# Performance work log

Hardware: AMD Instinct MI355X
Metric: run time of the kernel (lower is better)

The kernel has to match this reference:

```python
import jax, jax.numpy as jnp
import numpy as np

D = 1024       # num_feature == heads*dim_head
NHEADS = 16
HD = 64
INNER = NHEADS * HD
FF = 2048      # hardcoded mlp_dim in CSGO_model
L = 4          # depth
NOUT = 26      # hardcoded number of InvDynamic heads
IDH = 512      # inverse_dynamic_dim
B = 64
T = 32         # horizon


def _ln(x, g=None, b=None, eps=1e-5):
    mu = jnp.mean(x, axis=-1, keepdims=True)
    var = jnp.mean((x - mu) ** 2, axis=-1, keepdims=True)
    y = (x - mu) * jax.lax.rsqrt(var + eps)
    if g is not None:
        y = y * g + b
    return y


def setup_inputs() -> dict:
    key = jax.random.key(0)
    ks = jax.random.split(key, 20)
    s = 0.02
    inp = {
        'x': jax.random.normal(ks[0], (B, T, D), jnp.float32),
        # transformer params, stacked over depth L
        'qkv_w': jax.random.normal(ks[1], (L, D, 3 * INNER), jnp.float32) * s,
        'out_w': jax.random.normal(ks[2], (L, INNER, D), jnp.float32) * s,
        'out_b': jnp.zeros((L, D), jnp.float32),
        'attn_ln_g': jnp.ones((L, D), jnp.float32),
        'attn_ln_b': jnp.zeros((L, D), jnp.float32),
        'ff_ln_g': jnp.ones((L, D), jnp.float32),
        'ff_ln_b': jnp.zeros((L, D), jnp.float32),
        'ff_w1': jax.random.normal(ks[3], (L, D, FF), jnp.float32) * s,
        'ff_b1': jnp.zeros((L, FF), jnp.float32),
        'ff_w2': jax.random.normal(ks[4], (L, FF, D), jnp.float32) * s,
        'ff_b2': jnp.zeros((L, D), jnp.float32),
        # 26 InvDynamic heads, stacked
        'head_w1': jax.random.normal(ks[5], (NOUT, 2 * D, IDH), jnp.float32) * s,
        'head_b1': jnp.zeros((NOUT, IDH), jnp.float32),
        'head_w2': jax.random.normal(ks[6], (NOUT, IDH, IDH), jnp.float32) * s,
        'head_b2': jnp.zeros((NOUT, IDH), jnp.float32),
        'head_w3': jax.random.normal(ks[7], (NOUT, IDH, 1), jnp.float32) * s,
        'head_b3': jnp.zeros((NOUT, 1), jnp.float32),
    }
    return inp


def _forward(x, qkv_w, out_w, out_b, attn_ln_g, attn_ln_b, ff_ln_g, ff_ln_b,
             ff_w1, ff_b1, ff_w2, ff_b2,
             head_w1, head_b1, head_w2, head_b2, head_w3, head_b3):
    scale = HD ** -0.5

    def block(h, p):
        (qw, ow, ob, ag, ab, fg, fb, w1, b1, w2, b2) = p
        # x = attn(prenorm_ln(mid_ln(x))) + x  (mid LayerNorm has no affine, eps=1e-6)
        y = _ln(h, eps=1e-6)
        y = _ln(y, ag, ab)
        qkv = y @ qw                               # [B,T,3*INNER]
        q, k, v = jnp.split(qkv, 3, axis=-1)
        def split_heads(t):
            return t.reshape(t.shape[0], t.shape[1], NHEADS, HD).transpose(0, 2, 1, 3)
        q, k, v = split_heads(q), split_heads(k), split_heads(v)
        attn = jax.nn.softmax(jnp.einsum('bhqd,bhkd->bhqk', q, k) * scale, axis=-1)
        o = jnp.einsum('bhqk,bhkd->bhqd', attn, v)
        o = o.transpose(0, 2, 1, 3).reshape(h.shape[0], h.shape[1], INNER)
        h = h + (o @ ow + ob)
        # x = ff(prenorm_ln(x)) + x
        y = _ln(h, fg, fb)
        y = jax.nn.gelu(y @ w1 + b1, approximate=False) @ w2 + b2
        return h + y, None

    params = (qkv_w, out_w, out_b, attn_ln_g, attn_ln_b, ff_ln_g, ff_ln_b,
              ff_w1, ff_b1, ff_w2, ff_b2)
    x, _ = jax.lax.scan(block, x, params)

    # x_comb = concat(x[:,0], x[:,1])  -> [B, 2D]
    x_comb = jnp.concatenate([x[:, 0, :], x[:, 1, :]], axis=1)
    # 26 independent 3-layer MLP heads, batched as grouped GEMMs
    h1 = jax.nn.relu(jnp.einsum('bd,ndk->bnk', x_comb, head_w1) + head_b1)
    h2 = jax.nn.relu(jnp.einsum('bnk,nkj->bnj', h1, head_w2) + head_b2)
    out = jnp.einsum('bnk,nkj->bnj', h2, head_w3) + head_b3   # [B,26,1]
    return out


def reference(x, qkv_w, out_w, out_b, attn_ln_g, attn_ln_b, ff_ln_g, ff_ln_b,
              ff_w1, ff_b1, ff_w2, ff_b2,
              head_w1, head_b1, head_w2, head_b2, head_w3, head_b3):
    return _forward(x, qkv_w, out_w, out_b, attn_ln_g, attn_ln_b, ff_ln_g,
                    ff_ln_b, ff_w1, ff_b1, ff_w2, ff_b2,
                    head_w1, head_b1, head_w2, head_b2, head_w3, head_b3)
```

## Files before the change

kernel.cpp:

```cpp
#include <hip/hip_runtime.h>
#include <math.h>

static constexpr int BATCH = 64;
static constexpr int SEQ   = 32;
static constexpr int TOK   = BATCH * SEQ;
static constexpr int DIM   = 1024;
static constexpr int NH    = 16;
static constexpr int HDIM  = 64;
static constexpr int FFD   = 2048;
static constexpr int LAYERS= 4;
static constexpr int NHEAD_OUT = 26;
static constexpr int IDH   = 512;

typedef __bf16 bf16_t;
typedef __bf16 bf16x4 __attribute__((ext_vector_type(4)));
typedef __bf16 bf16x8 __attribute__((ext_vector_type(8)));
typedef float  f32x4  __attribute__((ext_vector_type(4)));
typedef float  f32x16 __attribute__((ext_vector_type(16)));
typedef unsigned short us4 __attribute__((ext_vector_type(4)));
typedef unsigned short us8 __attribute__((ext_vector_type(8)));

__device__ __forceinline__ unsigned short f2bfu(float f) {
    return __builtin_bit_cast(unsigned short, (bf16_t)f);
}

__device__ __forceinline__ void gload_lds16(const void* gp, void* lp) {
    __builtin_amdgcn_global_load_lds(
        (const __attribute__((address_space(1))) unsigned int*)gp,
        (__attribute__((address_space(3))) unsigned int*)lp,
        16, 0, 0);
}

__device__ __forceinline__ void tx_chunks4(const float* __restrict__ src,
                                           bf16_t* __restrict__ dst,
                                           int K, int N, int base4) {
    int nkb = K >> 6;
    int kk = threadIdx.x >> 6;
    int l  = threadIdx.x & 63;
    int nl = l & 31, k8 = (l >> 5) * 8;
    int base = base4 * 4;
    #pragma unroll
    for (int q = 0; q < 4; ++q) {
        int chunk = base + q;
        int ns = chunk / nkb;
        int kt = chunk - ns * nkb;
        int n = ns * 32 + nl;
        int kb = kt * 64 + kk * 16 + k8;
        us8 o;
        #pragma unroll
        for (int j = 0; j < 8; ++j)
            o[j] = f2bfu(src[(long)(kb + j) * N + n]);
        *(us8*)(dst + (long)chunk * 2048 + kk * 512 + l * 8) = o;
    }
}

__global__ __launch_bounds__(256) void txd1(const float* __restrict__ src,
                                            bf16_t* __restrict__ dst,
                                            int K, int N) {
    tx_chunks4(src, dst, K, N, blockIdx.x);
}

__device__ __forceinline__ float block_sum(float v, float* red) {
    #pragma unroll
    for (int off = 32; off > 0; off >>= 1) v += __shfl_down(v, off);
    int lane = threadIdx.x & 63;
    int w    = threadIdx.x >> 6;
    if (lane == 0) red[w] = v;
    __syncthreads();
    float t = red[0] + red[1] + red[2] + red[3];
    __syncthreads();
    return t;
}

template<bool PRE, bool F32IN>
__global__ __launch_bounds__(256) void ln_kernel(const void* __restrict__ xv,
                                                 const float* __restrict__ g,
                                                 const float* __restrict__ b,
                                                 bf16_t* __restrict__ y,
                                                 bf16_t* __restrict__ hout) {
    __shared__ float red[4];
    long row = blockIdx.x;
    int tid = threadIdx.x;
    float4 v;
    if (F32IN) {
        const float* xr = (const float*)xv + row * DIM;
        v = *(const float4*)(xr + tid * 4);
        us4 hc;
        hc.x = f2bfu(v.x); hc.y = f2bfu(v.y); hc.z = f2bfu(v.z); hc.w = f2bfu(v.w);
        *(us4*)(hout + row * DIM + tid * 4) = hc;
        v.x = (float)(bf16_t)v.x; v.y = (float)(bf16_t)v.y;
        v.z = (float)(bf16_t)v.z; v.w = (float)(bf16_t)v.w;
    } else {
        const bf16_t* xr = (const bf16_t*)xv + row * DIM;
        bf16x4 r4 = *(const bf16x4*)(xr + tid * 4);
        v.x = (float)r4[0]; v.y = (float)r4[1]; v.z = (float)r4[2]; v.w = (float)r4[3];
    }
    if (PRE) {
        float s  = block_sum(v.x + v.y + v.z + v.w, red);
        float mu = s * (1.0f / DIM);
        v.x -= mu; v.y -= mu; v.z -= mu; v.w -= mu;
        float ss = block_sum(v.x*v.x + v.y*v.y + v.z*v.z + v.w*v.w, red);
        float r  = 1.0f / sqrtf(ss * (1.0f / DIM) + 1e-6f);
        v.x *= r; v.y *= r; v.z *= r; v.w *= r;
    }
    float s  = block_sum(v.x + v.y + v.z + v.w, red);
    float mu = s * (1.0f / DIM);
    v.x -= mu; v.y -= mu; v.z -= mu; v.w -= mu;
    float ss = block_sum(v.x*v.x + v.y*v.y + v.z*v.z + v.w*v.w, red);
    float r  = 1.0f / sqrtf(ss * (1.0f / DIM) + 1e-5f);
    float4 gg = *(const float4*)(g + tid * 4);
    float4 bb = *(const float4*)(b + tid * 4);
    us4 o;
    o.x = f2bfu(v.x * r * gg.x + bb.x);
    o.y = f2bfu(v.y * r * gg.y + bb.y);
    o.z = f2bfu(v.z * r * gg.z + bb.z);
    o.w = f2bfu(v.w * r * gg.w + bb.w);
    *(us4*)(y + row * DIM + tid * 4) = o;
}

template<int BM, int BN, int WM, int WN, int EPI>
__global__ __launch_bounds__(256) void gemm32(
    const bf16_t* __restrict__ A, const bf16_t* __restrict__ BT,
    const float* __restrict__ bias, const bf16_t* __restrict__ resid,
    bf16_t* __restrict__ Ch,
    int N, int K, int gemmBlocks, int gx,
    const float* __restrict__ txsrc, bf16_t* __restrict__ txdst,
    int txK, int txN)
{
    constexpr int WAVES_N = BN / WN;
    constexpr int FM = WM / 32, FN = WN / 32;
    constexpr int NSTG = BM / 32 + BN / 32;

    __shared__ bf16_t As[2][BM * 64];
    __shared__ bf16_t Bs[2][BN * 64];

    int bid = blockIdx.x;
    if (bid >= gemmBlocks) {
        tx_chunks4(txsrc, txdst, txK, txN, bid - gemmBlocks);
        return;
    }
    int bx = bid % gx, by = bid / gx;

    int tid  = threadIdx.x;
    int wave = tid >> 6, lane = tid & 63;
    int wr = wave / WAVES_N, wc = wave % WAVES_N;
    int m0 = by * BM, n0 = bx * BN;

    f32x16 acc[FM][FN];
    #pragma unroll
    for (int m = 0; m < FM; ++m)
        #pragma unroll
        for (int n = 0; n < FN; ++n)
            #pragma unroll
            for (int r = 0; r < 16; ++r)
                acc[m][n][r] = 0.f;

    long rsb = (long)K * 2;
    int  lr  = lane & 31;
    int  lkb = (lane >> 5) * 16;
    int  nkb = K >> 6;

    const char* Abase = (const char*)A + (long)(m0 + lr) * rsb + lkb;
    const char* Bbase = (const char*)BT + (long)(n0 >> 5) * nkb * 4096 + lane * 16;

    auto stage = [&](int c, int t) {
        long kb = (long)t * 128;
        #pragma unroll
        for (int i = 0; i < BM / 32; ++i) {
            int b = i * 4 + wave;
            gload_lds16(Abase + (long)(b >> 2) * 32 * rsb + (b & 3) * 32 + kb,
                        (char*)&As[c][0] + b * 1024);
        }
        #pragma unroll
        for (int i = 0; i < BN / 32; ++i) {
            int b = i * 4 + wave;
            gload_lds16(Bbase + ((long)(b >> 2) * nkb + t) * 4096 + (b & 3) * 1024,
                        (char*)&Bs[c][0] + b * 1024);
        }
    };

    int nt = K >> 6;
    stage(0, 0);
    int cur = 0;
    for (int t = 0; t < nt; ++t) {
        if (t + 1 < nt) {
            stage(cur ^ 1, t + 1);
            asm volatile("s_waitcnt vmcnt(%c0)" :: "i"(NSTG) : "memory");
        } else {
            asm volatile("s_waitcnt vmcnt(0)" ::: "memory");
        }
        __builtin_amdgcn_s_barrier();
        asm volatile("" ::: "memory");
        bf16x8 af[FM][4], bq[FN][4];
        #pragma unroll
        for (int m = 0; m < FM; ++m)
            #pragma unroll
            for (int kk = 0; kk < 4; ++kk)
                af[m][kk] = *(const bf16x8*)((const char*)&As[cur][0] +
                            ((wr * FM + m) * 4 + kk) * 1024 + (lane << 4));
        #pragma unroll
        for (int n = 0; n < FN; ++n)
            #pragma unroll
            for (int kk = 0; kk < 4; ++kk)
                bq[n][kk] = *(const bf16x8*)((const char*)&Bs[cur][0] +
                            ((wc * FN + n) * 4 + kk) * 1024 + (lane << 4));
        #pragma unroll
        for (int kk = 0; kk < 4; ++kk)
            #pragma unroll
            for (int m = 0; m < FM; ++m)
                #pragma unroll
                for (int n = 0; n < FN; ++n)
                    acc[m][n] = __builtin_amdgcn_mfma_f32_32x32x16_bf16(
                        af[m][kk], bq[n][kk], acc[m][n], 0, 0, 0);
        asm volatile("" ::: "memory");
        __builtin_amdgcn_s_barrier();
        cur ^= 1;
    }

    int rbase = 4 * (lane >> 5);
    #pragma unroll
    for (int m = 0; m < FM; ++m) {
        #pragma unroll
        for (int n = 0; n < FN; ++n) {
            int colI = n0 + wc * WN + n * 32 + (lane & 31);
            float bb = (EPI != 0) ? bias[colI] : 0.f;
            #pragma unroll
            for (int r = 0; r < 16; ++r) {
                int rowI = m0 + wr * WM + m * 32 + rbase + (r & 3) + 8 * (r >> 2);
                float v = acc[m][n][r] + bb;
                if (EPI == 2) v = 0.5f * v * (1.0f + erff(v * 0.70710678118654752f));
                long off = (long)rowI * N + colI;
                if (EPI == 1) v += (float)resid[off];
                Ch[off] = (bf16_t)v;
            }
        }
    }
}

__global__ __launch_bounds__(256) void gemm_hd(
    const bf16_t* __restrict__ A, const float* __restrict__ Bw,
    const float* __restrict__ bias, bf16_t* __restrict__ C,
    int N, int K, long aStride, long sA, long sB, long sbias, long sC)
{
    long g = blockIdx.z;
    A += g * sA;
    const float* Bp = Bw + g * sB;
    bias += g * sbias;
    bf16_t* Cp = C + g * sC;

    __shared__ bf16_t As[2][64 * 64];
    __shared__ float  Bf[2][64 * 64];

    int tid = threadIdx.x, wave = tid >> 6, lane = tid & 63;
    int wr = wave >> 1, wc = wave & 1;
    int n0 = blockIdx.x * 64;

    f32x4 acc[2][2];
    #pragma unroll
    for (int m = 0; m < 2; ++m)
        #pragma unroll
        for (int n = 0; n < 2; ++n)
            acc[m][n] = f32x4{0.f, 0.f, 0.f, 0.f};

    long rsb = aStride * 2;
    int  lr  = lane & 15;
    int  lkb = (lane >> 4) * 16;
    const char* Abase = (const char*)A + (long)lr * rsb + lkb;

    auto stage = [&](int c, int t) {
        long kb = (long)t * 128;
        #pragma unroll
        for (int i = 0; i < 2; ++i) {
            int b = i * 4 + wave;
            gload_lds16(Abase + (long)(b >> 1) * 16 * rsb + (b & 1) * 64 + kb,
                        (char*)&As[c][0] + b * 1024);
        }
        #pragma unroll
        for (int i = 0; i < 4; ++i) {
            int ch = i * 4 + wave;
            int row = ch * 4 + (lane >> 4);
            gload_lds16((const char*)Bp + ((long)(t * 64 + row) * N + n0) * 4 + (lane & 15) * 16,
                        (char*)&Bf[c][0] + ch * 1024);
        }
    };

    int nt = K >> 6;
    stage(0, 0);
    int cur = 0;
    for (int t = 0; t < nt; ++t) {
        if (t + 1 < nt) {
            stage(cur ^ 1, t + 1);
            asm volatile("s_waitcnt vmcnt(6)" ::: "memory");
        } else {
            asm volatile("s_waitcnt vmcnt(0)" ::: "memory");
        }
        __builtin_amdgcn_s_barrier();
        asm volatile("" ::: "memory");
        bf16x8 af[2][2], bq[2][2];
        #pragma unroll
        for (int m = 0; m < 2; ++m)
            #pragma unroll
            for (int h = 0; h < 2; ++h)
                af[m][h] = *(const bf16x8*)((const char*)&As[cur][0] +
                           ((wr * 2 + m) * 2 + h) * 1024 + (lane << 4));
        #pragma unroll
        for (int n = 0; n < 2; ++n) {
            int nl = wc * 32 + n * 16 + lr;
            #pragma unroll
            for (int h = 0; h < 2; ++h) {
                #pragma unroll
                for (int j = 0; j < 8; ++j) {
                    float v = Bf[cur][(h * 32 + (lane >> 4) * 8 + j) * 64 + nl];
                    bq[n][h][j] = (bf16_t)v;
                }
            }
        }
        #pragma unroll
        for (int h = 0; h < 2; ++h)
            #pragma unroll
            for (int m = 0; m < 2; ++m)
                #pragma unroll
                for (int n = 0; n < 2; ++n)
                    acc[m][n] = __builtin_amdgcn_mfma_f32_16x16x32_bf16(
                        af[m][h], bq[n][h], acc[m][n], 0, 0, 0);
        asm volatile("" ::: "memory");
        __builtin_amdgcn_s_barrier();
        cur ^= 1;
    }

    int lq = (lane >> 4) * 4;
    #pragma unroll
    for (int m = 0; m < 2; ++m) {
        #pragma unroll
        for (int n = 0; n < 2; ++n) {
            int colI = n0 + wc * 32 + n * 16 + lr;
            float bb = bias[colI];
            #pragma unroll
            for (int j = 0; j < 4; ++j) {
                int rowI = wr * 32 + m * 16 + lq + j;
                float v = fmaxf(acc[m][n][j] + bb, 0.0f);
                Cp[(long)rowI * N + colI] = (bf16_t)v;
            }
        }
    }
}

__global__ __launch_bounds__(256) void attn_kernel(const bf16_t* __restrict__ qkv,
                                                   bf16_t* __restrict__ o) {
    int bh = blockIdx.x;
    int b  = bh >> 4;
    int hh = bh & 15;
    __shared__ float qs[32][65];
    __shared__ float kt[64][36];
    __shared__ float vs[32][68];
    __shared__ float ps[32][33];
    const bf16_t* base = qkv + (long)b * SEQ * (3 * DIM) + hh * HDIM;
    int tid = threadIdx.x;

    {
        int t = tid >> 3, c = (tid & 7) * 8;
        bf16x8 qv = *(const bf16x8*)(base + (long)t * 3 * DIM + c);
        bf16x8 kv = *(const bf16x8*)(base + (long)t * 3 * DIM + DIM + c);
        bf16x8 vv = *(const bf16x8*)(base + (long)t * 3 * DIM + 2 * DIM + c);
        #pragma unroll
        for (int j = 0; j < 8; ++j) {
            int d = c + j;
            qs[t][d] = (float)qv[j];
            kt[d][(((t >> 2) ^ ((d >> 2) & 7)) << 2) + (t & 3)] = (float)kv[j];
            vs[t][d] = (float)vv[j];
        }
    }
    __syncthreads();

    {
        int r  = tid >> 3;
        int c0 = (tid & 7) * 4;
        f32x4 acc = {0.f, 0.f, 0.f, 0.f};
        #pragma unroll
        for (int d = 0; d < 64; ++d) {
            float qv = qs[r][d];
            float4 kv = *(const float4*)&kt[d][(((c0 >> 2) ^ ((d >> 2) & 7)) << 2)];
            acc[0] = fmaf(qv, kv.x, acc[0]);
            acc[1] = fmaf(qv, kv.y, acc[1]);
            acc[2] = fmaf(qv, kv.z, acc[2]);
            acc[3] = fmaf(qv, kv.w, acc[3]);
        }
        #pragma unroll
        for (int i = 0; i < 4; ++i) ps[r][c0 + i] = acc[i] * 0.125f;
    }
    __syncthreads();

    if (tid < 32) {
        float mx = -1e30f;
        for (int c = 0; c < 32; ++c) mx = fmaxf(mx, ps[tid][c]);
        float sum = 0.f;
        for (int c = 0; c < 32; ++c) { float e = expf(ps[tid][c] - mx); ps[tid][c] = e; sum += e; }
        float inv = 1.f / sum;
        for (int c = 0; c < 32; ++c) ps[tid][c] *= inv;
    }
    __syncthreads();

    {
        int r  = tid >> 3;
        int d0 = (tid & 7) * 8;
        float acc[8] = {};
        #pragma unroll
        for (int c = 0; c < 32; ++c) {
            float pv = ps[r][c];
            float4 v0 = *(const float4*)&vs[c][d0];
            float4 v1 = *(const float4*)&vs[c][d0 + 4];
            acc[0] = fmaf(pv, v0.x, acc[0]);
            acc[1] = fmaf(pv, v0.y, acc[1]);
            acc[2] = fmaf(pv, v0.z, acc[2]);
            acc[3] = fmaf(pv, v0.w, acc[3]);
            acc[4] = fmaf(pv, v1.x, acc[4]);
            acc[5] = fmaf(pv, v1.y, acc[5]);
            acc[6] = fmaf(pv, v1.z, acc[6]);
            acc[7] = fmaf(pv, v1.w, acc[7]);
        }
        us8 ov;
        #pragma unroll
        for (int j = 0; j < 8; ++j) ov[j] = f2bfu(acc[j]);
        *(us8*)(o + (long)b * SEQ * DIM + (long)r * DIM + hh * HDIM + d0) = ov;
    }
}

__global__ __launch_bounds__(256) void head3_kernel(const bf16_t* __restrict__ h2,
                                                    const float* __restrict__ w3,
                                                    const float* __restrict__ b3,
                                                    float* __restrict__ out) {
    int gid  = blockIdx.x * 256 + threadIdx.x;
    int wave = gid >> 6;
    int lane = gid & 63;
    if (wave >= NHEAD_OUT * BATCH) return;
    int n = wave >> 6;
    int b = wave & 63;
    const bf16_t* a = h2 + ((long)n * BATCH + b) * IDH;
    const float*  w = w3 + (long)n * IDH;
    float acc = 0.f;
    #pragma unroll
    for (int i = lane; i < IDH; i += 64) acc = fmaf((float)a[i], w[i], acc);
    #pragma unroll
    for (int off = 32; off > 0; off >>= 1) acc += __shfl_down(acc, off);
    if (lane == 0) out[b * NHEAD_OUT + n] = acc + b3[n];
}

extern "C" void kernel_launch(void* const* d_in, const int* in_sizes, int n_in,
                              void* d_out, int out_size, void* d_ws, size_t ws_size,
                              hipStream_t stream) {
    const float* x      = (const float*)d_in[0];
    const float* qkv_w  = (const float*)d_in[1];
    const float* out_w  = (const float*)d_in[2];
    const float* out_b  = (const float*)d_in[3];
    const float* attn_g = (const float*)d_in[4];
    const float* attn_b = (const float*)d_in[5];
    const float* ff_g   = (const float*)d_in[6];
    const float* ff_b   = (const float*)d_in[7];
    const float* ff_w1  = (const float*)d_in[8];
    const float* ff_b1  = (const float*)d_in[9];
    const float* ff_w2  = (const float*)d_in[10];
    const float* ff_b2  = (const float*)d_in[11];
    const float* hw1    = (const float*)d_in[12];
    const float* hb1    = (const float*)d_in[13];
    const float* hw2    = (const float*)d_in[14];
    const float* hb2    = (const float*)d_in[15];
    const float* hw3    = (const float*)d_in[16];
    const float* hb3    = (const float*)d_in[17];
    float* out = (float*)d_out;

    char* p = (char*)d_ws;
    bf16_t* h     = (bf16_t*)p;           p += (long)TOK * DIM * 2;
    bf16_t* qkvb  = (bf16_t*)p;           p += (long)TOK * 3 * DIM * 2;
    bf16_t* y     = (bf16_t*)p;           p += (long)TOK * DIM * 2;
    bf16_t* ob    = (bf16_t*)p;           p += (long)TOK * DIM * 2;
    bf16_t* ffb   = (bf16_t*)p;           p += (long)TOK * FFD * 2;
    bf16_t* h1    = (bf16_t*)p;           p += (long)NHEAD_OUT * BATCH * IDH * 2;
    bf16_t* h2    = (bf16_t*)p;           p += (long)NHEAD_OUT * BATCH * IDH * 2;
    bf16_t* qkvwt = (bf16_t*)p;           p += (long)LAYERS * DIM * 3 * DIM * 2;
    bf16_t* outwt = (bf16_t*)p;           p += (long)LAYERS * DIM * DIM * 2;
    bf16_t* ff1t  = (bf16_t*)p;           p += (long)LAYERS * DIM * FFD * 2;
    bf16_t* ff2t  = (bf16_t*)p;           p += (long)LAYERS * FFD * DIM * 2;

    const long sQ = (long)DIM * 3 * DIM;
    const long sO = (long)DIM * DIM;
    const long sF1 = (long)DIM * FFD;
    const long sF2 = (long)FFD * DIM;
    const int tbQ  = (3 * DIM / 32) * (DIM / 64) / 4;
    const int tbO  = (DIM / 32) * (DIM / 64) / 4;
    const int tbF1 = (FFD / 32) * (DIM / 64) / 4;
    const int tbF2 = (DIM / 32) * (FFD / 64) / 4;

    txd1<<<tbQ, 256, 0, stream>>>(qkv_w, qkvwt, DIM, 3 * DIM);

    for (int l = 0; l < LAYERS; ++l) {
        bool more = (l + 1 < LAYERS);
        if (l == 0)
            ln_kernel<true, true><<<TOK, 256, 0, stream>>>(
                x, attn_g, attn_b, y, h);
        else
            ln_kernel<true, false><<<TOK, 256, 0, stream>>>(
                h, attn_g + l * DIM, attn_b + l * DIM, y, nullptr);

        {
            int gx = 3 * DIM / 128, gb = gx * (TOK / 64);
            gemm32<64, 128, 32, 64, 0><<<gb + tbO, 256, 0, stream>>>(
                y, qkvwt + l * sQ, nullptr, nullptr, qkvb,
                3 * DIM, DIM, gb, gx,
                out_w + l * sO, outwt + l * sO, DIM, DIM);
        }
        attn_kernel<<<BATCH * NH, 256, 0, stream>>>(qkvb, ob);
        {
            int gx = DIM / 64, gb = gx * (TOK / 64);
            gemm32<64, 64, 32, 32, 1><<<gb + tbF1, 256, 0, stream>>>(
                ob, outwt + l * sO, out_b + l * DIM, h, h,
                DIM, DIM, gb, gx,
                ff_w1 + l * sF1, ff1t + l * sF1, DIM, FFD);
        }
        ln_kernel<false, false><<<TOK, 256, 0, stream>>>(
            h, ff_g + l * DIM, ff_b + l * DIM, y, nullptr);
        {
            int gx = FFD / 128, gb = gx * (TOK / 64);
            gemm32<64, 128, 32, 64, 2><<<gb + tbF2, 256, 0, stream>>>(
                y, ff1t + l * sF1, ff_b1 + l * FFD, nullptr, ffb,
                FFD, DIM, gb, gx,
                ff_w2 + l * sF2, ff2t + l * sF2, FFD, DIM);
        }
        {
            int gx = DIM / 64, gb = gx * (TOK / 64);
            gemm32<64, 64, 32, 32, 1><<<gb + (more ? tbQ : 0), 256, 0, stream>>>(
                ffb, ff2t + l * sF2, ff_b2 + l * DIM, h, h,
                DIM, FFD, gb, gx,
                qkv_w + (l + 1) * sQ, qkvwt + (l + 1) * sQ, DIM, 3 * DIM);
        }
    }

    gemm_hd<<<dim3(IDH / 64, 1, NHEAD_OUT), 256, 0, stream>>>(
        h, hw1, hb1, h1,
        IDH, 2 * DIM, (long)SEQ * DIM,
        0, (long)2 * DIM * IDH, IDH, (long)BATCH * IDH);
    gemm_hd<<<dim3(IDH / 64, 1, NHEAD_OUT), 256, 0, stream>>>(
        h1, hw2, hb2, h2,
        IDH, IDH, IDH,
        (long)BATCH * IDH, (long)IDH * IDH, IDH, (long)BATCH * IDH);
    head3_kernel<<<(NHEAD_OUT * BATCH * 64) / 256, 256, 0, stream>>>(h2, hw3, hb3, out);
}
```

Measured before the change: 515.0 us.

## Pre-convert head weights to bf16 in spare blocks of transformer GEMM launches

Adds extra blocks to each transformer GEMM launch that convert the fp32 InvDynamic head weights (w1, w2) to bf16 in chunks, spread across the 16 launches. The head GEMMs then stream bf16 weights, which halves their global and LDS traffic and removes the in-loop float-to-bf16 conversion. The conversion is still done every call, but it overlaps with the GEMM tails. It adds workspace and more blocks per GEMM launch, which could delay the GEMMs.

```diff
diff --git a/kernel.cpp b/kernel.cpp
--- a/kernel.cpp
+++ b/kernel.cpp
@@ -12,6 +12,9 @@
 static constexpr int NHEAD_OUT = 26;
 static constexpr int IDH   = 512;
 
+static constexpr int HB1 = (NHEAD_OUT * 2 * DIM * IDH) / 8192;
+static constexpr int HB2 = (NHEAD_OUT * IDH * IDH) / 8192;
+
 typedef __bf16 bf16_t;
 typedef __bf16 bf16x4 __attribute__((ext_vector_type(4)));
 typedef __bf16 bf16x8 __attribute__((ext_vector_type(8)));
@@ -51,6 +54,22 @@
         for (int j = 0; j < 8; ++j)
             o[j] = f2bfu(src[(long)(kb + j) * N + n]);
         *(us8*)(dst + (long)chunk * 2048 + kk * 512 + l * 8) = o;
+    }
+}
+
+__device__ __forceinline__ void cvt_chunk8k(const float* __restrict__ src,
+                                            bf16_t* __restrict__ dst,
+                                            int blk) {
+    long base = (long)blk * 8192 + threadIdx.x * 8;
+    #pragma unroll
+    for (int i = 0; i < 4; ++i) {
+        long off = base + (long)i * 2048;
+        float4 a = *(const float4*)(src + off);
+        float4 b = *(const float4*)(src + off + 4);
+        us8 o;
+        o[0] = f2bfu(a.x); o[1] = f2bfu(a.y); o[2] = f2bfu(a.z); o[3] = f2bfu(a.w);
+        o[4] = f2bfu(b.x); o[5] = f2bfu(b.y); o[6] = f2bfu(b.z); o[7] = f2bfu(b.w);
+        *(us8*)(dst + off) = o;
     }
 }
 
@@ -125,7 +144,10 @@
     bf16_t* __restrict__ Ch,
     int N, int K, int gemmBlocks, int gx,
     const float* __restrict__ txsrc, bf16_t* __restrict__ txdst,
-    int txK, int txN)
+    int txK, int txN, int txCnt,
+    const float* __restrict__ hs1, bf16_t* __restrict__ hd1,
+    const float* __restrict__ hs2, bf16_t* __restrict__ hd2,
+    int headBase)
 {
     constexpr int WAVES_N = BN / WN;
     constexpr int FM = WM / 32, FN = WN / 32;
@@ -136,7 +158,14 @@
 
     int bid = blockIdx.x;
     if (bid >= gemmBlocks) {
-        tx_chunks4(txsrc, txdst, txK, txN, bid - gemmBlocks);
+        int t2 = bid - gemmBlocks;
+        if (t2 < txCnt) {
+            tx_chunks4(txsrc, txdst, txK, txN, t2);
+        } else {
+            int hIdx = headBase + (t2 - txCnt);
+            if (hIdx < HB1) cvt_chunk8k(hs1, hd1, hIdx);
+            else            cvt_chunk8k(hs2, hd2, hIdx - HB1);
+        }
         return;
     }
     int bx = bid % gx, by = bid / gx;
@@ -238,18 +267,18 @@
 }
 
 __global__ __launch_bounds__(256) void gemm_hd(
-    const bf16_t* __restrict__ A, const float* __restrict__ Bw,
+    const bf16_t* __restrict__ A, const bf16_t* __restrict__ Bw,
     const float* __restrict__ bias, bf16_t* __restrict__ C,
     int N, int K, long aStride, long sA, long sB, long sbias, long sC)
 {
     long g = blockIdx.z;
     A += g * sA;
-    const float* Bp = Bw + g * sB;
+    const char* Bp = (const char*)(Bw + g * sB);
     bias += g * sbias;
     bf16_t* Cp = C + g * sC;
 
     __shared__ bf16_t As[2][64 * 64];
-    __shared__ float  Bf[2][64 * 64];
+    __shared__ bf16_t Bf[2][64 * 64];
 
     int tid = threadIdx.x, wave = tid >> 6, lane = tid & 63;
     int wr = wave >> 1, wc = wave & 1;
@@ -276,10 +305,10 @@
                         (char*)&As[c][0] + b * 1024);
         }
         #pragma unroll
-        for (int i = 0; i < 4; ++i) {
+        for (int i = 0; i < 2; ++i) {
             int ch = i * 4 + wave;
-            int row = ch * 4 + (lane >> 4);
-            gload_lds16((const char*)Bp + ((long)(t * 64 + row) * N + n0) * 4 + (lane & 15) * 16,
+            int row = ch * 8 + (lane >> 3);
+            gload_lds16(Bp + ((long)(t * 64 + row) * N + n0) * 2 + (lane & 7) * 16,
                         (char*)&Bf[c][0] + ch * 1024);
         }
     };
@@ -290,7 +319,7 @@
     for (int t = 0; t < nt; ++t) {
         if (t + 1 < nt) {
             stage(cur ^ 1, t + 1);
-            asm volatile("s_waitcnt vmcnt(6)" ::: "memory");
+            asm volatile("s_waitcnt vmcnt(4)" ::: "memory");
         } else {
             asm volatile("s_waitcnt vmcnt(0)" ::: "memory");
         }
@@ -309,10 +338,8 @@
             #pragma unroll
             for (int h = 0; h < 2; ++h) {
                 #pragma unroll
-                for (int j = 0; j < 8; ++j) {
-                    float v = Bf[cur][(h * 32 + (lane >> 4) * 8 + j) * 64 + nl];
-                    bq[n][h][j] = (bf16_t)v;
-                }
+                for (int j = 0; j < 8; ++j)
+                    bq[n][h][j] = Bf[cur][(h * 32 + (lane >> 4) * 8 + j) * 64 + nl];
             }
         }
         #pragma unroll
@@ -480,6 +507,8 @@
     bf16_t* outwt = (bf16_t*)p;           p += (long)LAYERS * DIM * DIM * 2;
     bf16_t* ff1t  = (bf16_t*)p;           p += (long)LAYERS * DIM * FFD * 2;
     bf16_t* ff2t  = (bf16_t*)p;           p += (long)LAYERS * FFD * DIM * 2;
+    bf16_t* hw1b  = (bf16_t*)p;           p += (long)NHEAD_OUT * 2 * DIM * IDH * 2;
+    bf16_t* hw2b  = (bf16_t*)p;           p += (long)NHEAD_OUT * IDH * IDH * 2;
 
     const long sQ = (long)DIM * 3 * DIM;
     const long sO = (long)DIM * DIM;
@@ -489,6 +518,8 @@
     const int tbO  = (DIM / 32) * (DIM / 64) / 4;
     const int tbF1 = (FFD / 32) * (DIM / 64) / 4;
     const int tbF2 = (DIM / 32) * (FFD / 64) / 4;
+    const int HCNT = (HB1 + HB2) / 16;
+    int headOff = 0;
 
     txd1<<<tbQ, 256, 0, stream>>>(qkv_w, qkvwt, DIM, 3 * DIM);
 
@@ -503,43 +534,52 @@
 
         {
             int gx = 3 * DIM / 128, gb = gx * (TOK / 64);
-            gemm32<64, 128, 32, 64, 0><<<gb + tbO, 256, 0, stream>>>(
+            gemm32<64, 128, 32, 64, 0><<<gb + tbO + HCNT, 256, 0, stream>>>(
                 y, qkvwt + l * sQ, nullptr, nullptr, qkvb,
                 3 * DIM, DIM, gb, gx,
-                out_w + l * sO, outwt + l * sO, DIM, DIM);
+                out_w + l * sO, outwt + l * sO, DIM, DIM, tbO,
+                hw1, hw1b, hw2, hw2b, headOff);
+            headOff += HCNT;
         }
         attn_kernel<<<BATCH * NH, 256, 0, stream>>>(qkvb, ob);
         {
             int gx = DIM / 64, gb = gx * (TOK / 64);
-            gemm32<64, 64, 32, 32, 1><<<gb + tbF1, 256, 0, stream>>>(
+            gemm32<64, 64, 32, 32, 1><<<gb + tbF1 + HCNT, 256, 0, stream>>>(
                 ob, outwt + l * sO, out_b + l * DIM, h, h,
                 DIM, DIM, gb, gx,
-                ff_w1 + l * sF1, ff1t + l * sF1, DIM, FFD);
+                ff_w1 + l * sF1, ff1t + l * sF1, DIM, FFD, tbF1,
+                hw1, hw1b, hw2, hw2b, headOff);
+            headOff += HCNT;
         }
         ln_kernel<false, false><<<TOK, 256, 0, stream>>>(
             h, ff_g + l * DIM, ff_b + l * DIM, y, nullptr);
         {
             int gx = FFD / 128, gb = gx * (TOK / 64);
-            gemm32<64, 128, 32, 64, 2><<<gb + tbF2, 256, 0, stream>>>(
+            gemm32<64, 128, 32, 64, 2><<<gb + tbF2 + HCNT, 256, 0, stream>>>(
                 y, ff1t + l * sF1, ff_b1 + l * FFD, nullptr, ffb,
                 FFD, DIM, gb, gx,
-                ff_w2 + l * sF2, ff2t + l * sF2, FFD, DIM);
+                ff_w2 + l * sF2, ff2t + l * sF2, FFD, DIM, tbF2,
+                hw1, hw1b, hw2, hw2b, headOff);
+            headOff += HCNT;
         }
         {
             int gx = DIM / 64, gb = gx * (TOK / 64);
-            gemm32<64, 64, 32, 32, 1><<<gb + (more ? tbQ : 0), 256, 0, stream>>>(
+            int tc = more ? tbQ : 0;
+            gemm32<64, 64, 32, 32, 1><<<gb + tc + HCNT, 256, 0, stream>>>(
                 ffb, ff2t + l * sF2, ff_b2 + l * DIM, h, h,
                 DIM, FFD, gb, gx,
-                qkv_w + (l + 1) * sQ, qkvwt + (l + 1) * sQ, DIM, 3 * DIM);
+                qkv_w + (l + 1) * sQ, qkvwt + (l + 1) * sQ, DIM, 3 * DIM, tc,
+                hw1, hw1b, hw2, hw2b, headOff);
+            headOff += HCNT;
         }
     }
 
     gemm_hd<<<dim3(IDH / 64, 1, NHEAD_OUT), 256, 0, stream>>>(
-        h, hw1, hb1, h1,
+        h, hw1b, hb1, h1,
         IDH, 2 * DIM, (long)SEQ * DIM,
         0, (long)2 * DIM * IDH, IDH, (long)BATCH * IDH);
     gemm_hd<<<dim3(IDH / 64, 1, NHEAD_OUT), 256, 0, stream>>>(
-        h1, hw2, hb2, h2,
+        h1, hw2b, hb2, h2,
         IDH, IDH, IDH,
         (long)BATCH * IDH, (long)IDH * IDH, IDH, (long)BATCH * IDH);
     head3_kernel<<<(NHEAD_OUT * BATCH * 64) / 256, 256, 0, stream>>>(h2, hw3, hb3, out);
```

Measured after the change: 533.5 us. 1.04x slower.
